# Performance work log

Hardware: AMD Instinct MI355X
Metric: run time of the kernel (lower is better)

The kernel has to match this reference:

```python
import jax, jax.numpy as jnp
import numpy as np

N = 50000  # nodes


def gcn_layer(x, src, dst, W, b):
    """DGL GraphConv with norm='both': D_in^{-1/2} A^T D_out^{-1/2} x W + b."""
    E = src.shape[0]
    ones = jnp.ones((E,), dtype=x.dtype)
    deg_out = jax.ops.segment_sum(ones, src, num_segments=N)  # out-degree of src nodes
    deg_in = jax.ops.segment_sum(ones, dst, num_segments=N)   # in-degree of dst nodes
    norm_src = jax.lax.rsqrt(jnp.maximum(deg_out, 1.0))
    norm_dst = jax.lax.rsqrt(jnp.maximum(deg_in, 1.0))
    h = x * norm_src[:, None]
    agg = jax.ops.segment_sum(h[src], dst, num_segments=N)  # [N, in_dim]
    return (agg @ W) * norm_dst[:, None] + b


def encoder(feat, src, dst, W1, b1, W2, b2):
    h = jax.nn.relu(gcn_layer(feat, src, dst, W1, b1))
    h = jax.nn.relu(gcn_layer(h, src, dst, W2, b2))
    return h


def proj(h, fc1_W, fc1_b, fc2_W, fc2_b):
    z = jax.nn.elu(h @ fc1_W + fc1_b)
    return z @ fc2_W + fc2_b


def setup_inputs() -> dict:
    key = jax.random.key(0)
    ks = jax.random.split(key, 12)
    in_dim, hid, out_dim, E = 128, 128, 128, 800000
    inp = {
        "feat1": jax.random.normal(ks[0], (N, in_dim), dtype=jnp.float32),
        "feat2": jax.random.normal(ks[1], (N, in_dim), dtype=jnp.float32),
        "edge_index1": jax.random.randint(ks[2], (2, E), 0, N),
        "edge_index2": jax.random.randint(ks[3], (2, E), 0, N),
        # GraphConv weights: in_dim -> 2*hid -> hid
        "conv1_W": jax.random.normal(ks[4], (in_dim, 2 * hid), dtype=jnp.float32) * 0.05,
        "conv1_b": jnp.zeros((2 * hid,), dtype=jnp.float32),
        "conv2_W": jax.random.normal(ks[5], (2 * hid, hid), dtype=jnp.float32) * 0.05,
        "conv2_b": jnp.zeros((hid,), dtype=jnp.float32),
        # MLP proj: fc1 hid->out, fc2 out->hid
        "fc1_W": jax.random.normal(ks[6], (hid, out_dim), dtype=jnp.float32) * 0.05,
        "fc1_b": jnp.zeros((out_dim,), dtype=jnp.float32),
        "fc2_W": jax.random.normal(ks[7], (out_dim, hid), dtype=jnp.float32) * 0.05,
        "fc2_b": jnp.zeros((hid,), dtype=jnp.float32),
    }
    return inp


def reference(feat1, feat2, edge_index1, edge_index2,
              conv1_W, conv1_b, conv2_W, conv2_b,
              fc1_W, fc1_b, fc2_W, fc2_b):
    h1 = encoder(feat1, edge_index1[0], edge_index1[1], conv1_W, conv1_b, conv2_W, conv2_b)
    h2 = encoder(feat2, edge_index2[0], edge_index2[1], conv1_W, conv1_b, conv2_W, conv2_b)
    z1 = proj(h1, fc1_W, fc1_b, fc2_W, fc2_b)
    z2 = proj(h2, fc1_W, fc1_b, fc2_W, fc2_b)
    return (z1, z2)
```

## Files before the change

### kernel.cpp

```cpp
#include <hip/hip_runtime.h>
#include <math.h>

#define NDIM 128
#define H2   256
#define MAXG 2
#define TPE  8192
#define NBKMAX 512

typedef __attribute__((ext_vector_type(8))) short bf16x8;
typedef __attribute__((ext_vector_type(4))) float f32x4;

__device__ __forceinline__ unsigned short f2bf(float f) {
    unsigned int u = __float_as_uint(f);
    u += 0x7fffu + ((u >> 16) & 1u);
    return (unsigned short)(u >> 16);
}
__device__ __forceinline__ float bf2f(unsigned short h) {
    return __uint_as_float(((unsigned int)h) << 16);
}
__device__ __forceinline__ void split2(float f, unsigned short& h, unsigned short& l) {
    h = f2bf(f);
    l = f2bf(f - bf2f(h));
}

struct BinArgs {
    const int* src[MAXG]; const int* dst[MAXG];
    int* histD[MAXG]; int* histS[MAXG];
    int* totD[MAXG];  int* baseD[MAXG];
    int* totS[MAXG];  int* baseS[MAXG];
    unsigned int* pairs[MAXG];
    unsigned short* srcS[MAXG];
    float* ns[MAXG];
    int E[MAXG]; int NBK; int NT; int n;
};

__global__ __launch_bounds__(256) void binA(BinArgs a) {
    __shared__ int cntD[NBKMAX], cntS[NBKMAX];
    int g = blockIdx.y, t = blockIdx.x, tid = threadIdx.x;
    for (int b = tid; b < NBKMAX; b += 256) { cntD[b] = 0; cntS[b] = 0; }
    __syncthreads();
    int E = a.E[g];
    int base = t * TPE;
#pragma unroll
    for (int k = 0; k < TPE / 256; ++k) {
        int e = base + k * 256 + tid;
        if (e < E) {
            atomicAdd(&cntD[a.dst[g][e] >> 7], 1);
            atomicAdd(&cntS[a.src[g][e] >> 7], 1);
        }
    }
    __syncthreads();
    for (int b = tid; b < a.NBK; b += 256) {
        a.histD[g][t * a.NBK + b] = cntD[b];
        a.histS[g][t * a.NBK + b] = cntS[b];
    }
}

__global__ void binB1(BinArgs a) {
    int g = blockIdx.y, side = blockIdx.z;
    int b = blockIdx.x * 256 + threadIdx.x;
    if (b >= a.NBK) return;
    const int* hist = side ? a.histS[g] : a.histD[g];
    int s = 0;
    for (int t = 0; t < a.NT; ++t) s += hist[t * a.NBK + b];
    (side ? a.totS[g] : a.totD[g])[b] = s;
}

__global__ __launch_bounds__(512) void binB2(BinArgs a) {
    int g = blockIdx.y, side = blockIdx.z;
    __shared__ int s[512];
    int t = threadIdx.x;
    const int* tot = side ? a.totS[g] : a.totD[g];
    int v = (t < a.NBK) ? tot[t] : 0;
    s[t] = v;
    __syncthreads();
    for (int off = 1; off < 512; off <<= 1) {
        int u = (t >= off) ? s[t - off] : 0;
        __syncthreads();
        s[t] += u;
        __syncthreads();
    }
    if (t < a.NBK) (side ? a.baseS[g] : a.baseD[g])[t] = s[t] - v;
}

__global__ void binB3(BinArgs a) {
    int g = blockIdx.y, side = blockIdx.z;
    int b = blockIdx.x * 64 + threadIdx.x;
    if (b >= a.NBK) return;
    int* hist = side ? a.histS[g] : a.histD[g];
    int run = (side ? a.baseS[g] : a.baseD[g])[b];
    for (int t = 0; t < a.NT; ++t) {
        int v = hist[t * a.NBK + b];
        hist[t * a.NBK + b] = run;
        run += v;
    }
}

__global__ __launch_bounds__(256) void binC(BinArgs a) {
    __shared__ int offD[NBKMAX], offS[NBKMAX];
    int g = blockIdx.y, t = blockIdx.x, tid = threadIdx.x;
    for (int b = tid; b < a.NBK; b += 256) {
        offD[b] = a.histD[g][t * a.NBK + b];
        offS[b] = a.histS[g][t * a.NBK + b];
    }
    __syncthreads();
    int E = a.E[g];
    int base = t * TPE;
    unsigned int* pairs = a.pairs[g];
    unsigned short* ss = a.srcS[g];
#pragma unroll
    for (int k = 0; k < TPE / 256; ++k) {
        int e = base + k * 256 + tid;
        if (e < E) {
            int s = a.src[g][e], d = a.dst[g][e];
            int pos = atomicAdd(&offD[d >> 7], 1);
            pairs[pos] = ((unsigned int)(d & 127) << 16) | (unsigned int)s;
            int posS = atomicAdd(&offS[s >> 7], 1);
            ss[posS] = (unsigned short)s;
        }
    }
}

__global__ __launch_bounds__(256) void srchist(BinArgs a) {
    __shared__ int cnt[128];
    int g = blockIdx.y, b = blockIdx.x, tid = threadIdx.x;
    if (tid < 128) cnt[tid] = 0;
    __syncthreads();
    int base = a.baseS[g][b], tot = a.totS[g][b];
    const unsigned short* ss = a.srcS[g];
    for (int i = tid; i < tot; i += 256)
        atomicAdd(&cnt[ss[base + i] & 127], 1);
    __syncthreads();
    if (tid < 128) {
        int node = b * 128 + tid;
        if (node < a.n) {
            int c = cnt[tid];
            a.ns[g][node] = rsqrtf((float)(c > 1 ? c : 1));
        }
    }
}

struct SortArgs {
    const unsigned int* pairs[MAXG];
    const int* totD[MAXG]; const int* baseD[MAXG];
    int* row_ptr[MAXG]; int* row_end[MAXG];
    int* edge_srt[MAXG];
    float* nd[MAXG];
    int n;
};

__global__ __launch_bounds__(256) void bucket_sort(SortArgs a) {
    __shared__ int hist[128], scan[128], cur[128];
    int g = blockIdx.y, bkt = blockIdx.x, tid = threadIdx.x;
    if (tid < 128) hist[tid] = 0;
    __syncthreads();
    int cnt = a.totD[g][bkt], base = a.baseD[g][bkt];
    const unsigned int* pp = a.pairs[g] + base;
    for (int i = tid; i < cnt; i += 256) atomicAdd(&hist[pp[i] >> 16], 1);
    __syncthreads();
    if (tid < 128) scan[tid] = hist[tid];
    __syncthreads();
    for (int off = 1; off < 128; off <<= 1) {
        int v = (tid < 128 && tid >= off) ? scan[tid - off] : 0;
        __syncthreads();
        if (tid < 128) scan[tid] += v;
        __syncthreads();
    }
    if (tid < 128) {
        int incl = scan[tid];
        int h = hist[tid];
        cur[tid] = incl - h;
        int node = bkt * 128 + tid;
        if (node < a.n) {
            a.row_ptr[g][node] = base + incl - h;
            a.row_end[g][node] = base + incl;
            a.nd[g][node] = rsqrtf((float)(h > 1 ? h : 1));
        }
    }
    __syncthreads();
    for (int i = tid; i < cnt; i += 256) {
        unsigned int p = pp[i];
        int pos = atomicAdd(&cur[p >> 16], 1);
        a.edge_srt[g][base + pos] = (int)(p & 0xFFFF);
    }
}

struct GatherArgs {
    const float* X[MAXG];
    const int* row_ptr[MAXG]; const int* row_end[MAXG]; const int* edge_src[MAXG];
    const float* ns[MAXG]; const float* nd[MAXG];
    unsigned short* outH[MAXG]; unsigned short* outL[MAXG];
    const float* bias; int use_nd; int relu_on; int n;
};

__global__ __launch_bounds__(256) void gather_split_b(GatherArgs a) {
    int g = blockIdx.y;
    int half = threadIdx.x >> 5;
    int lane = threadIdx.x & 31;
    int r = blockIdx.x * 8 + half;
    if (r >= a.n) return;
    int j = a.row_ptr[g][r];
    int end = a.row_end[g][r];
    const int* ep = a.edge_src[g];
    const float* X = a.X[g];
    const float* rs = a.ns[g];
    int base = lane * 4;
    float4 acc = make_float4(0.f, 0.f, 0.f, 0.f);
    for (; j + 3 < end; j += 4) {
        int s0 = ep[j], s1 = ep[j + 1], s2 = ep[j + 2], s3 = ep[j + 3];
        float c0 = rs[s0], c1 = rs[s1], c2 = rs[s2], c3 = rs[s3];
        float4 v0 = *(const float4*)(X + (size_t)s0 * NDIM + base);
        float4 v1 = *(const float4*)(X + (size_t)s1 * NDIM + base);
        float4 v2 = *(const float4*)(X + (size_t)s2 * NDIM + base);
        float4 v3 = *(const float4*)(X + (size_t)s3 * NDIM + base);
        acc.x += v0.x * c0 + v1.x * c1 + v2.x * c2 + v3.x * c3;
        acc.y += v0.y * c0 + v1.y * c1 + v2.y * c2 + v3.y * c3;
        acc.z += v0.z * c0 + v1.z * c1 + v2.z * c2 + v3.z * c3;
        acc.w += v0.w * c0 + v1.w * c1 + v2.w * c2 + v3.w * c3;
    }
    for (; j < end; ++j) {
        int s0 = ep[j];
        float c0 = rs[s0];
        float4 v0 = *(const float4*)(X + (size_t)s0 * NDIM + base);
        acc.x += v0.x * c0; acc.y += v0.y * c0;
        acc.z += v0.z * c0; acc.w += v0.w * c0;
    }
    float v[4] = {acc.x, acc.y, acc.z, acc.w};
    if (a.use_nd) {
        float s = a.nd[g][r];
#pragma unroll
        for (int i = 0; i < 4; ++i) {
            v[i] = v[i] * s + a.bias[base + i];
            if (a.relu_on) v[i] = fmaxf(v[i], 0.f);
        }
    }
    unsigned short h[4], l[4];
#pragma unroll
    for (int i = 0; i < 4; ++i) split2(v[i], h[i], l[i]);
    *(ushort4*)(a.outH[g] + (size_t)r * NDIM + base) = make_ushort4(h[0], h[1], h[2], h[3]);
    *(ushort4*)(a.outL[g] + (size_t)r * NDIM + base) = make_ushort4(l[0], l[1], l[2], l[3]);
}

__global__ void wprep_all(const float* __restrict__ W1, const float* __restrict__ W2,
                          const float* __restrict__ F1, const float* __restrict__ F2,
                          unsigned short* __restrict__ W1h, unsigned short* __restrict__ W1l,
                          unsigned short* __restrict__ W2h, unsigned short* __restrict__ W2l,
                          unsigned short* __restrict__ F1h, unsigned short* __restrict__ F1l,
                          unsigned short* __restrict__ F2h, unsigned short* __restrict__ F2l) {
    int i = blockIdx.x * 256 + threadIdx.x;
    const float* Wsrc; unsigned short *Hd, *Ld; int K, Nc, idx;
    if (i < 32768)       { Wsrc = W1; Hd = W1h; Ld = W1l; K = 128; Nc = 256; idx = i; }
    else if (i < 65536)  { Wsrc = W2; Hd = W2h; Ld = W2l; K = 256; Nc = 128; idx = i - 32768; }
    else if (i < 81920)  { Wsrc = F1; Hd = F1h; Ld = F1l; K = 128; Nc = 128; idx = i - 65536; }
    else                 { Wsrc = F2; Hd = F2h; Ld = F2l; K = 128; Nc = 128; idx = i - 81920; }
    int k = idx / Nc, n = idx % Nc;
    unsigned short h, l;
    split2(Wsrc[idx], h, l);
    Hd[n * K + k] = h;
    Ld[n * K + k] = l;
}

struct GemmArgs {
    const unsigned short* Ah[MAXG]; const unsigned short* Al[MAXG];
    const unsigned short* Bh; const unsigned short* Bl;
    float* C[MAXG]; unsigned short* CH[MAXG]; unsigned short* CL[MAXG];
    const float* rsOut[MAXG]; const float* bOut;
    int M, K, Nc, act, has_rs, has_b, split_out;
};

__global__ __launch_bounds__(256) void mfma_gemm_b(GemmArgs a) {
    __shared__ __align__(16) unsigned short Ah[64 * 40];
    __shared__ __align__(16) unsigned short Al[64 * 40];
    __shared__ __align__(16) unsigned short Bh[128 * 40];
    __shared__ __align__(16) unsigned short Bl[128 * 40];

    int g = blockIdx.z;
    const unsigned short* Ah_g = a.Ah[g];
    const unsigned short* Al_g = a.Al[g];

    int tid  = threadIdx.x;
    int wave = tid >> 6, lane = tid & 63;
    int quad = lane >> 4, l16 = lane & 15;
    int rowBase = blockIdx.x * 64;
    int colBase = blockIdx.y * 128;
    int M = a.M, K = a.K, Nc = a.Nc;

    f32x4 acc[4][2] = {};

    int s_row   = tid >> 2;
    int s_chunk = (tid & 3) * 8;

    for (int k0 = 0; k0 < K; k0 += 32) {
        int gr = rowBase + s_row;
        uint4 va_h = make_uint4(0, 0, 0, 0), va_l = make_uint4(0, 0, 0, 0);
        if (gr < M) {
            va_h = *(const uint4*)(Ah_g + (size_t)gr * K + k0 + s_chunk);
            va_l = *(const uint4*)(Al_g + (size_t)gr * K + k0 + s_chunk);
        }
        *(uint4*)(Ah + s_row * 40 + s_chunk) = va_h;
        *(uint4*)(Al + s_row * 40 + s_chunk) = va_l;
#pragma unroll
        for (int c = tid; c < 512; c += 256) {
            int bn = c >> 2, bc = (c & 3) * 8;
            uint4 vb_h = *(const uint4*)(a.Bh + (size_t)(colBase + bn) * K + k0 + bc);
            uint4 vb_l = *(const uint4*)(a.Bl + (size_t)(colBase + bn) * K + k0 + bc);
            *(uint4*)(Bh + bn * 40 + bc) = vb_h;
            *(uint4*)(Bl + bn * 40 + bc) = vb_l;
        }
        __syncthreads();

        bf16x8 af[4], alf[4], bhf[2], blf[2];
#pragma unroll
        for (int i = 0; i < 4; ++i) {
            af[i]  = *(const bf16x8*)(Ah + (i * 16 + l16) * 40 + quad * 8);
            alf[i] = *(const bf16x8*)(Al + (i * 16 + l16) * 40 + quad * 8);
        }
#pragma unroll
        for (int j = 0; j < 2; ++j) {
            bhf[j] = *(const bf16x8*)(Bh + (wave * 32 + j * 16 + l16) * 40 + quad * 8);
            blf[j] = *(const bf16x8*)(Bl + (wave * 32 + j * 16 + l16) * 40 + quad * 8);
        }
#pragma unroll
        for (int i = 0; i < 4; ++i)
#pragma unroll
            for (int j = 0; j < 2; ++j) {
                acc[i][j] = __builtin_amdgcn_mfma_f32_16x16x32_bf16(af[i],  bhf[j], acc[i][j], 0, 0, 0);
                acc[i][j] = __builtin_amdgcn_mfma_f32_16x16x32_bf16(alf[i], bhf[j], acc[i][j], 0, 0, 0);
                acc[i][j] = __builtin_amdgcn_mfma_f32_16x16x32_bf16(af[i],  blf[j], acc[i][j], 0, 0, 0);
            }
        __syncthreads();
    }

#pragma unroll
    for (int i = 0; i < 4; ++i) {
#pragma unroll
        for (int r = 0; r < 4; ++r) {
            int row = rowBase + i * 16 + quad * 4 + r;
            if (row >= M) continue;
            float rs = a.has_rs ? a.rsOut[g][row] : 1.0f;
#pragma unroll
            for (int j = 0; j < 2; ++j) {
                int col = colBase + wave * 32 + j * 16 + l16;
                float v = acc[i][j][r] * rs;
                if (a.has_b) v += a.bOut[col];
                if (a.act == 1) v = fmaxf(v, 0.f);
                else if (a.act == 2) v = v > 0.f ? v : expm1f(v);
                if (a.split_out) {
                    unsigned short h, l;
                    split2(v, h, l);
                    a.CH[g][(size_t)row * Nc + col] = h;
                    a.CL[g][(size_t)row * Nc + col] = l;
                } else {
                    a.C[g][(size_t)row * Nc + col] = v;
                }
            }
        }
    }
}

extern "C" void kernel_launch(void* const* d_in, const int* in_sizes, int n_in,
                              void* d_out, int out_size, void* d_ws, size_t ws_size,
                              hipStream_t stream) {
    const float* feat[2] = {(const float*)d_in[0], (const float*)d_in[1]};
    const int*   ei[2]   = {(const int*)d_in[2], (const int*)d_in[3]};
    const float* W1   = (const float*)d_in[4];
    const float* b1   = (const float*)d_in[5];
    const float* W2   = (const float*)d_in[6];
    const float* b2   = (const float*)d_in[7];
    const float* fc1W = (const float*)d_in[8];
    const float* fc1b = (const float*)d_in[9];
    const float* fc2W = (const float*)d_in[10];
    const float* fc2b = (const float*)d_in[11];
    int N = in_sizes[0] / NDIM;
    float* out = (float*)d_out;

    int Emax = 0;
    for (int g = 0; g < 2; ++g) { int E = in_sizes[2 + g] / 2; if (E > Emax) Emax = E; }
    int NBK = (N + 127) / 128;
    int NT  = (Emax + TPE - 1) / TPE;

    char* p = (char*)d_ws;
    float* ns_[2]; float* nd_[2];
    for (int i = 0; i < 2; ++i) { ns_[i] = (float*)p; p += (size_t)N * 4; }
    for (int i = 0; i < 2; ++i) { nd_[i] = (float*)p; p += (size_t)N * 4; }
    int* rp_[2]; int* re_[2]; int* esrt_[2];
    for (int i = 0; i < 2; ++i) { rp_[i] = (int*)p; p += (size_t)N * 4; }
    for (int i = 0; i < 2; ++i) { re_[i] = (int*)p; p += (size_t)N * 4; }
    for (int i = 0; i < 2; ++i) { esrt_[i] = (int*)p; p += (size_t)Emax * 4; }
    unsigned short* R1[2]; unsigned short* R2[2];
    for (int i = 0; i < 2; ++i) { R1[i] = (unsigned short*)p; p += (size_t)N * NDIM * 2 * 2; }
    for (int i = 0; i < 2; ++i) { R2[i] = (unsigned short*)p; p += (size_t)N * H2 * 2 * 2; }
    unsigned short* W1th = (unsigned short*)p; p += (size_t)NDIM * H2 * 2;
    unsigned short* W1tl = (unsigned short*)p; p += (size_t)NDIM * H2 * 2;
    unsigned short* W2th = (unsigned short*)p; p += (size_t)H2 * NDIM * 2;
    unsigned short* W2tl = (unsigned short*)p; p += (size_t)H2 * NDIM * 2;
    unsigned short* f1th = (unsigned short*)p; p += (size_t)NDIM * NDIM * 2;
    unsigned short* f1tl = (unsigned short*)p; p += (size_t)NDIM * NDIM * 2;
    unsigned short* f2th = (unsigned short*)p; p += (size_t)NDIM * NDIM * 2;
    unsigned short* f2tl = (unsigned short*)p; p += (size_t)NDIM * NDIM * 2;
    int* tb = (int*)p; p += (size_t)2 * 4 * NBK * 4;

    int* histD_[2]; int* histS_[2]; unsigned int* pairs_[2]; unsigned short* srcS_[2];
    for (int i = 0; i < 2; ++i) {
        histD_[i] = (int*)R2[i];
        histS_[i] = (int*)R2[i] + (size_t)NT * NBK;
        pairs_[i] = (unsigned int*)((char*)R2[i] + (1 << 20));
        srcS_[i]  = (unsigned short*)R1[i];
    }

    BinArgs ba = {};
    ba.NBK = NBK; ba.NT = NT; ba.n = N;
    for (int i = 0; i < 2; ++i) {
        int E = in_sizes[2 + i] / 2;
        ba.src[i] = ei[i]; ba.dst[i] = ei[i] + E; ba.E[i] = E;
        ba.histD[i] = histD_[i]; ba.histS[i] = histS_[i];
        ba.totD[i]  = tb + (size_t)i * 4 * NBK;
        ba.baseD[i] = tb + (size_t)i * 4 * NBK + NBK;
        ba.totS[i]  = tb + (size_t)i * 4 * NBK + 2 * NBK;
        ba.baseS[i] = tb + (size_t)i * 4 * NBK + 3 * NBK;
        ba.pairs[i] = pairs_[i]; ba.srcS[i] = srcS_[i];
        ba.ns[i] = ns_[i];
    }

    wprep_all<<<384, 256, 0, stream>>>(W1, W2, fc1W, fc2W,
                                       W1th, W1tl, W2th, W2tl, f1th, f1tl, f2th, f2tl);
    binA<<<dim3(NT, 2), 256, 0, stream>>>(ba);
    binB1<<<dim3((NBK + 255) / 256, 2, 2), 256, 0, stream>>>(ba);
    binB2<<<dim3(1, 2, 2), 512, 0, stream>>>(ba);
    binB3<<<dim3((NBK + 63) / 64, 2, 2), 64, 0, stream>>>(ba);
    binC<<<dim3(NT, 2), 256, 0, stream>>>(ba);
    srchist<<<dim3(NBK, 2), 256, 0, stream>>>(ba);

    SortArgs sa = {};
    sa.n = N;
    for (int i = 0; i < 2; ++i) {
        sa.pairs[i] = pairs_[i];
        sa.totD[i] = ba.totD[i]; sa.baseD[i] = ba.baseD[i];
        sa.row_ptr[i] = rp_[i]; sa.row_end[i] = re_[i];
        sa.edge_srt[i] = esrt_[i]; sa.nd[i] = nd_[i];
    }
    bucket_sort<<<dim3(NBK, 2), 256, 0, stream>>>(sa);

    unsigned short *A1h[2], *A1l[2], *X1h[2], *X1l[2], *Gh[2], *Gl[2], *Zh[2], *Zl[2];
    float* T[2];
    for (int i = 0; i < 2; ++i) {
        A1h[i] = R1[i]; A1l[i] = R1[i] + (size_t)N * NDIM;
        T[i]   = (float*)R1[i];
        Zh[i]  = R1[i]; Zl[i]  = R1[i] + (size_t)N * NDIM;
        X1h[i] = R2[i]; X1l[i] = R2[i] + (size_t)N * H2;
        Gh[i]  = R2[i]; Gl[i]  = R2[i] + (size_t)N * NDIM;
    }

    int ggrid = (N + 7) / 8;
    int mgrid = (N + 63) / 64;

    GatherArgs ga = {};
    ga.n = N; ga.use_nd = 0; ga.relu_on = 0; ga.bias = b2;
    for (int i = 0; i < 2; ++i) {
        ga.X[i] = feat[i];
        ga.row_ptr[i] = rp_[i]; ga.row_end[i] = re_[i]; ga.edge_src[i] = esrt_[i];
        ga.ns[i] = ns_[i]; ga.nd[i] = nd_[i];
        ga.outH[i] = A1h[i]; ga.outL[i] = A1l[i];
    }
    gather_split_b<<<dim3(ggrid, 2), 256, 0, stream>>>(ga);

    GemmArgs g1 = {};
    g1.Bh = W1th; g1.Bl = W1tl; g1.bOut = b1;
    g1.M = N; g1.K = NDIM; g1.Nc = H2; g1.act = 1; g1.has_rs = 1; g1.has_b = 1; g1.split_out = 1;
    for (int i = 0; i < 2; ++i) {
        g1.Ah[i] = A1h[i]; g1.Al[i] = A1l[i];
        g1.CH[i] = X1h[i]; g1.CL[i] = X1l[i]; g1.rsOut[i] = nd_[i];
    }
    mfma_gemm_b<<<dim3(mgrid, H2 / 128, 2), 256, 0, stream>>>(g1);

    GemmArgs g2 = {};
    g2.Bh = W2th; g2.Bl = W2tl;
    g2.M = N; g2.K = H2; g2.Nc = NDIM; g2.act = 0; g2.has_rs = 0; g2.has_b = 0; g2.split_out = 0;
    for (int i = 0; i < 2; ++i) { g2.Ah[i] = X1h[i]; g2.Al[i] = X1l[i]; g2.C[i] = T[i]; }
    mfma_gemm_b<<<dim3(mgrid, 1, 2), 256, 0, stream>>>(g2);

    GatherArgs gb = ga;
    gb.use_nd = 1; gb.relu_on = 1;
    for (int i = 0; i < 2; ++i) {
        gb.X[i] = T[i];
        gb.outH[i] = Gh[i]; gb.outL[i] = Gl[i];
    }
    gather_split_b<<<dim3(ggrid, 2), 256, 0, stream>>>(gb);

    GemmArgs g3 = {};
    g3.Bh = f1th; g3.Bl = f1tl; g3.bOut = fc1b;
    g3.M = N; g3.K = NDIM; g3.Nc = NDIM; g3.act = 2; g3.has_rs = 0; g3.has_b = 1; g3.split_out = 1;
    for (int i = 0; i < 2; ++i) {
        g3.Ah[i] = Gh[i]; g3.Al[i] = Gl[i];
        g3.CH[i] = Zh[i]; g3.CL[i] = Zl[i];
    }
    mfma_gemm_b<<<dim3(mgrid, 1, 2), 256, 0, stream>>>(g3);

    GemmArgs g4 = {};
    g4.Bh = f2th; g4.Bl = f2tl; g4.bOut = fc2b;
    g4.M = N; g4.K = NDIM; g4.Nc = NDIM; g4.act = 0; g4.has_rs = 0; g4.has_b = 1; g4.split_out = 0;
    for (int i = 0; i < 2; ++i) {
        g4.Ah[i] = Zh[i]; g4.Al[i] = Zl[i];
        g4.C[i] = out + (size_t)i * N * NDIM;
    }
    mfma_gemm_b<<<dim3(mgrid, 1, 2), 256, 0, stream>>>(g4);
}
```

Measured before the change: 636.1 us.

## Fuse binning/sort kernels, prescale source norm, use 16-bit edge indices

Merges the three bin-scan kernels into one and the source-degree histogram with the bucket sort into one finalize kernel, cutting launches. The source normalization is applied once per node, by a prescale pass for layer one and by the second GEMM epilogue for layer two. This removes per-edge norm lookups from the gather. Sorted edge indices are stored as 16-bit values to halve index traffic, at the cost of an extra full feature pass for prescaling.

```diff
diff --git a/kernel.cpp b/kernel.cpp
--- a/kernel.cpp
+++ b/kernel.cpp
@@ -30,7 +30,6 @@
     int* totS[MAXG];  int* baseS[MAXG];
     unsigned int* pairs[MAXG];
     unsigned short* srcS[MAXG];
-    float* ns[MAXG];
     int E[MAXG]; int NBK; int NT; int n;
 };
 
@@ -56,43 +55,34 @@
     }
 }
 
-__global__ void binB1(BinArgs a) {
+__global__ __launch_bounds__(512) void binB(BinArgs a) {
     int g = blockIdx.y, side = blockIdx.z;
-    int b = blockIdx.x * 256 + threadIdx.x;
-    if (b >= a.NBK) return;
-    const int* hist = side ? a.histS[g] : a.histD[g];
-    int s = 0;
-    for (int t = 0; t < a.NT; ++t) s += hist[t * a.NBK + b];
-    (side ? a.totS[g] : a.totD[g])[b] = s;
-}
-
-__global__ __launch_bounds__(512) void binB2(BinArgs a) {
-    int g = blockIdx.y, side = blockIdx.z;
+    int* hist = side ? a.histS[g] : a.histD[g];
+    int* tot  = side ? a.totS[g]  : a.totD[g];
+    int* base = side ? a.baseS[g] : a.baseD[g];
     __shared__ int s[512];
-    int t = threadIdx.x;
-    const int* tot = side ? a.totS[g] : a.totD[g];
-    int v = (t < a.NBK) ? tot[t] : 0;
-    s[t] = v;
+    int b = threadIdx.x;
+    int v = 0;
+    if (b < a.NBK)
+        for (int t = 0; t < a.NT; ++t) v += hist[t * a.NBK + b];
+    s[b] = v;
     __syncthreads();
     for (int off = 1; off < 512; off <<= 1) {
-        int u = (t >= off) ? s[t - off] : 0;
+        int u = (b >= off) ? s[b - off] : 0;
         __syncthreads();
-        s[t] += u;
+        s[b] += u;
         __syncthreads();
     }
-    if (t < a.NBK) (side ? a.baseS[g] : a.baseD[g])[t] = s[t] - v;
-}
-
-__global__ void binB3(BinArgs a) {
-    int g = blockIdx.y, side = blockIdx.z;
-    int b = blockIdx.x * 64 + threadIdx.x;
-    if (b >= a.NBK) return;
-    int* hist = side ? a.histS[g] : a.histD[g];
-    int run = (side ? a.baseS[g] : a.baseD[g])[b];
-    for (int t = 0; t < a.NT; ++t) {
-        int v = hist[t * a.NBK + b];
-        hist[t * a.NBK + b] = run;
-        run += v;
+    int excl = s[b] - v;
+    if (b < a.NBK) {
+        tot[b] = v;
+        base[b] = excl;
+        int run = excl;
+        for (int t = 0; t < a.NT; ++t) {
+            int h = hist[t * a.NBK + b];
+            hist[t * a.NBK + b] = run;
+            run += h;
+        }
     }
 }
 
@@ -121,53 +111,50 @@
     }
 }
 
-__global__ __launch_bounds__(256) void srchist(BinArgs a) {
-    __shared__ int cnt[128];
-    int g = blockIdx.y, b = blockIdx.x, tid = threadIdx.x;
-    if (tid < 128) cnt[tid] = 0;
-    __syncthreads();
-    int base = a.baseS[g][b], tot = a.totS[g][b];
-    const unsigned short* ss = a.srcS[g];
-    for (int i = tid; i < tot; i += 256)
-        atomicAdd(&cnt[ss[base + i] & 127], 1);
+struct FinArgs {
+    const unsigned int* pairs[MAXG];
+    const unsigned short* srcS[MAXG];
+    const int* totD[MAXG]; const int* baseD[MAXG];
+    const int* totS[MAXG]; const int* baseS[MAXG];
+    int* row_ptr[MAXG]; int* row_end[MAXG];
+    unsigned short* edge_srt[MAXG];
+    float* ns[MAXG]; float* nd[MAXG];
+    int n;
+};
+
+__global__ __launch_bounds__(256) void finalize(FinArgs a) {
+    __shared__ int cnt[128], hist[128], scn[128], cur[128];
+    int g = blockIdx.y, bkt = blockIdx.x, tid = threadIdx.x;
+    if (tid < 128) { cnt[tid] = 0; hist[tid] = 0; }
+    __syncthreads();
+    {
+        int base = a.baseS[g][bkt], tot = a.totS[g][bkt];
+        const unsigned short* ss = a.srcS[g];
+        for (int i = tid; i < tot; i += 256)
+            atomicAdd(&cnt[ss[base + i] & 127], 1);
+    }
+    int cntE = a.totD[g][bkt], base = a.baseD[g][bkt];
+    const unsigned int* pp = a.pairs[g] + base;
+    for (int i = tid; i < cntE; i += 256)
+        atomicAdd(&hist[pp[i] >> 16], 1);
     __syncthreads();
     if (tid < 128) {
-        int node = b * 128 + tid;
+        int node = bkt * 128 + tid;
         if (node < a.n) {
             int c = cnt[tid];
             a.ns[g][node] = rsqrtf((float)(c > 1 ? c : 1));
         }
-    }
-}
-
-struct SortArgs {
-    const unsigned int* pairs[MAXG];
-    const int* totD[MAXG]; const int* baseD[MAXG];
-    int* row_ptr[MAXG]; int* row_end[MAXG];
-    int* edge_srt[MAXG];
-    float* nd[MAXG];
-    int n;
-};
-
-__global__ __launch_bounds__(256) void bucket_sort(SortArgs a) {
-    __shared__ int hist[128], scan[128], cur[128];
-    int g = blockIdx.y, bkt = blockIdx.x, tid = threadIdx.x;
-    if (tid < 128) hist[tid] = 0;
-    __syncthreads();
-    int cnt = a.totD[g][bkt], base = a.baseD[g][bkt];
-    const unsigned int* pp = a.pairs[g] + base;
-    for (int i = tid; i < cnt; i += 256) atomicAdd(&hist[pp[i] >> 16], 1);
-    __syncthreads();
-    if (tid < 128) scan[tid] = hist[tid];
+        scn[tid] = hist[tid];
+    }
     __syncthreads();
     for (int off = 1; off < 128; off <<= 1) {
-        int v = (tid < 128 && tid >= off) ? scan[tid - off] : 0;
+        int v = (tid < 128 && tid >= off) ? scn[tid - off] : 0;
         __syncthreads();
-        if (tid < 128) scan[tid] += v;
+        if (tid < 128) scn[tid] += v;
         __syncthreads();
     }
     if (tid < 128) {
-        int incl = scan[tid];
+        int incl = scn[tid];
         int h = hist[tid];
         cur[tid] = incl - h;
         int node = bkt * 128 + tid;
@@ -178,19 +165,33 @@
         }
     }
     __syncthreads();
-    for (int i = tid; i < cnt; i += 256) {
+    for (int i = tid; i < cntE; i += 256) {
         unsigned int p = pp[i];
         int pos = atomicAdd(&cur[p >> 16], 1);
-        a.edge_srt[g][base + pos] = (int)(p & 0xFFFF);
-    }
+        a.edge_srt[g][base + pos] = (unsigned short)(p & 0xFFFF);
+    }
+}
+
+struct PreArgs { const float* X[MAXG]; const float* ns[MAXG]; float* Xs[MAXG]; int n; };
+
+__global__ __launch_bounds__(256) void prescale(PreArgs a) {
+    int g = blockIdx.y;
+    int i = blockIdx.x * 256 + threadIdx.x;
+    if (i >= a.n * 32) return;
+    int row = i >> 5;
+    float s = a.ns[g][row];
+    float4 v = ((const float4*)a.X[g])[i];
+    v.x *= s; v.y *= s; v.z *= s; v.w *= s;
+    ((float4*)a.Xs[g])[i] = v;
 }
 
 struct GatherArgs {
     const float* X[MAXG];
-    const int* row_ptr[MAXG]; const int* row_end[MAXG]; const int* edge_src[MAXG];
-    const float* ns[MAXG]; const float* nd[MAXG];
+    const int* row_ptr[MAXG]; const int* row_end[MAXG];
+    const unsigned short* edge_src[MAXG];
+    const float* nd[MAXG];
     unsigned short* outH[MAXG]; unsigned short* outL[MAXG];
-    const float* bias; int use_nd; int relu_on; int n;
+    const float* bias; int use_nd; int n;
 };
 
 __global__ __launch_bounds__(256) void gather_split_b(GatherArgs a) {
@@ -201,38 +202,32 @@
     if (r >= a.n) return;
     int j = a.row_ptr[g][r];
     int end = a.row_end[g][r];
-    const int* ep = a.edge_src[g];
+    const unsigned short* ep = a.edge_src[g];
     const float* X = a.X[g];
-    const float* rs = a.ns[g];
     int base = lane * 4;
     float4 acc = make_float4(0.f, 0.f, 0.f, 0.f);
     for (; j + 3 < end; j += 4) {
         int s0 = ep[j], s1 = ep[j + 1], s2 = ep[j + 2], s3 = ep[j + 3];
-        float c0 = rs[s0], c1 = rs[s1], c2 = rs[s2], c3 = rs[s3];
         float4 v0 = *(const float4*)(X + (size_t)s0 * NDIM + base);
         float4 v1 = *(const float4*)(X + (size_t)s1 * NDIM + base);
         float4 v2 = *(const float4*)(X + (size_t)s2 * NDIM + base);
         float4 v3 = *(const float4*)(X + (size_t)s3 * NDIM + base);
-        acc.x += v0.x * c0 + v1.x * c1 + v2.x * c2 + v3.x * c3;
-        acc.y += v0.y * c0 + v1.y * c1 + v2.y * c2 + v3.y * c3;
-        acc.z += v0.z * c0 + v1.z * c1 + v2.z * c2 + v3.z * c3;
-        acc.w += v0.w * c0 + v1.w * c1 + v2.w * c2 + v3.w * c3;
+        acc.x += v0.x + v1.x + v2.x + v3.x;
+        acc.y += v0.y + v1.y + v2.y + v3.y;
+        acc.z += v0.z + v1.z + v2.z + v3.z;
+        acc.w += v0.w + v1.w + v2.w + v3.w;
     }
     for (; j < end; ++j) {
         int s0 = ep[j];
-        float c0 = rs[s0];
         float4 v0 = *(const float4*)(X + (size_t)s0 * NDIM + base);
-        acc.x += v0.x * c0; acc.y += v0.y * c0;
-        acc.z += v0.z * c0; acc.w += v0.w * c0;
+        acc.x += v0.x; acc.y += v0.y; acc.z += v0.z; acc.w += v0.w;
     }
     float v[4] = {acc.x, acc.y, acc.z, acc.w};
     if (a.use_nd) {
         float s = a.nd[g][r];
 #pragma unroll
-        for (int i = 0; i < 4; ++i) {
-            v[i] = v[i] * s + a.bias[base + i];
-            if (a.relu_on) v[i] = fmaxf(v[i], 0.f);
-        }
+        for (int i = 0; i < 4; ++i)
+            v[i] = fmaxf(v[i] * s + a.bias[base + i], 0.f);
     }
     unsigned short h[4], l[4];
 #pragma unroll
@@ -383,10 +378,10 @@
     float* ns_[2]; float* nd_[2];
     for (int i = 0; i < 2; ++i) { ns_[i] = (float*)p; p += (size_t)N * 4; }
     for (int i = 0; i < 2; ++i) { nd_[i] = (float*)p; p += (size_t)N * 4; }
-    int* rp_[2]; int* re_[2]; int* esrt_[2];
+    int* rp_[2]; int* re_[2]; unsigned short* esrt_[2];
     for (int i = 0; i < 2; ++i) { rp_[i] = (int*)p; p += (size_t)N * 4; }
     for (int i = 0; i < 2; ++i) { re_[i] = (int*)p; p += (size_t)N * 4; }
-    for (int i = 0; i < 2; ++i) { esrt_[i] = (int*)p; p += (size_t)Emax * 4; }
+    for (int i = 0; i < 2; ++i) { esrt_[i] = (unsigned short*)p; p += (size_t)Emax * 2; }
     unsigned short* R1[2]; unsigned short* R2[2];
     for (int i = 0; i < 2; ++i) { R1[i] = (unsigned short*)p; p += (size_t)N * NDIM * 2 * 2; }
     for (int i = 0; i < 2; ++i) { R2[i] = (unsigned short*)p; p += (size_t)N * H2 * 2 * 2; }
@@ -401,11 +396,13 @@
     int* tb = (int*)p; p += (size_t)2 * 4 * NBK * 4;
 
     int* histD_[2]; int* histS_[2]; unsigned int* pairs_[2]; unsigned short* srcS_[2];
+    float* Xs_[2];
     for (int i = 0; i < 2; ++i) {
         histD_[i] = (int*)R2[i];
         histS_[i] = (int*)R2[i] + (size_t)NT * NBK;
         pairs_[i] = (unsigned int*)((char*)R2[i] + (1 << 20));
         srcS_[i]  = (unsigned short*)R1[i];
+        Xs_[i]    = (float*)R2[i];
     }
 
     BinArgs ba = {};
@@ -419,27 +416,30 @@
         ba.totS[i]  = tb + (size_t)i * 4 * NBK + 2 * NBK;
         ba.baseS[i] = tb + (size_t)i * 4 * NBK + 3 * NBK;
         ba.pairs[i] = pairs_[i]; ba.srcS[i] = srcS_[i];
-        ba.ns[i] = ns_[i];
     }
 
     wprep_all<<<384, 256, 0, stream>>>(W1, W2, fc1W, fc2W,
                                        W1th, W1tl, W2th, W2tl, f1th, f1tl, f2th, f2tl);
     binA<<<dim3(NT, 2), 256, 0, stream>>>(ba);
-    binB1<<<dim3((NBK + 255) / 256, 2, 2), 256, 0, stream>>>(ba);
-    binB2<<<dim3(1, 2, 2), 512, 0, stream>>>(ba);
-    binB3<<<dim3((NBK + 63) / 64, 2, 2), 64, 0, stream>>>(ba);
+    binB<<<dim3(1, 2, 2), 512, 0, stream>>>(ba);
     binC<<<dim3(NT, 2), 256, 0, stream>>>(ba);
-    srchist<<<dim3(NBK, 2), 256, 0, stream>>>(ba);
-
-    SortArgs sa = {};
-    sa.n = N;
-    for (int i = 0; i < 2; ++i) {
-        sa.pairs[i] = pairs_[i];
-        sa.totD[i] = ba.totD[i]; sa.baseD[i] = ba.baseD[i];
-        sa.row_ptr[i] = rp_[i]; sa.row_end[i] = re_[i];
-        sa.edge_srt[i] = esrt_[i]; sa.nd[i] = nd_[i];
-    }
-    bucket_sort<<<dim3(NBK, 2), 256, 0, stream>>>(sa);
+
+    FinArgs fa = {};
+    fa.n = N;
+    for (int i = 0; i < 2; ++i) {
+        fa.pairs[i] = pairs_[i]; fa.srcS[i] = srcS_[i];
+        fa.totD[i] = ba.totD[i]; fa.baseD[i] = ba.baseD[i];
+        fa.totS[i] = ba.totS[i]; fa.baseS[i] = ba.baseS[i];
+        fa.row_ptr[i] = rp_[i]; fa.row_end[i] = re_[i];
+        fa.edge_srt[i] = esrt_[i];
+        fa.ns[i] = ns_[i]; fa.nd[i] = nd_[i];
+    }
+    finalize<<<dim3(NBK, 2), 256, 0, stream>>>(fa);
+
+    PreArgs pa = {};
+    pa.n = N;
+    for (int i = 0; i < 2; ++i) { pa.X[i] = feat[i]; pa.ns[i] = ns_[i]; pa.Xs[i] = Xs_[i]; }
+    prescale<<<dim3((N * 32 + 255) / 256, 2), 256, 0, stream>>>(pa);
 
     unsigned short *A1h[2], *A1l[2], *X1h[2], *X1l[2], *Gh[2], *Gl[2], *Zh[2], *Zl[2];
     float* T[2];
@@ -455,11 +455,11 @@
     int mgrid = (N + 63) / 64;
 
     GatherArgs ga = {};
-    ga.n = N; ga.use_nd = 0; ga.relu_on = 0; ga.bias = b2;
-    for (int i = 0; i < 2; ++i) {
-        ga.X[i] = feat[i];
+    ga.n = N; ga.use_nd = 0; ga.bias = b2;
+    for (int i = 0; i < 2; ++i) {
+        ga.X[i] = Xs_[i];
         ga.row_ptr[i] = rp_[i]; ga.row_end[i] = re_[i]; ga.edge_src[i] = esrt_[i];
-        ga.ns[i] = ns_[i]; ga.nd[i] = nd_[i];
+        ga.nd[i] = nd_[i];
         ga.outH[i] = A1h[i]; ga.outL[i] = A1l[i];
     }
     gather_split_b<<<dim3(ggrid, 2), 256, 0, stream>>>(ga);
@@ -475,12 +475,14 @@
 
     GemmArgs g2 = {};
     g2.Bh = W2th; g2.Bl = W2tl;
-    g2.M = N; g2.K = H2; g2.Nc = NDIM; g2.act = 0; g2.has_rs = 0; g2.has_b = 0; g2.split_out = 0;
-    for (int i = 0; i < 2; ++i) { g2.Ah[i] = X1h[i]; g2.Al[i] = X1l[i]; g2.C[i] = T[i]; }
+    g2.M = N; g2.K = H2; g2.Nc = NDIM; g2.act = 0; g2.has_rs = 1; g2.has_b = 0; g2.split_out = 0;
+    for (int i = 0; i < 2; ++i) {
+        g2.Ah[i] = X1h[i]; g2.Al[i] = X1l[i]; g2.C[i] = T[i]; g2.rsOut[i] = ns_[i];
+    }
     mfma_gemm_b<<<dim3(mgrid, 1, 2), 256, 0, stream>>>(g2);
 
     GatherArgs gb = ga;
-    gb.use_nd = 1; gb.relu_on = 1;
+    gb.use_nd = 1;
     for (int i = 0; i < 2; ++i) {
         gb.X[i] = T[i];
         gb.outH[i] = Gh[i]; gb.outL[i] = Gl[i];
```

After: 633.9 us. About the same (-0.3%).
